# Optimization experiments

Hardware: AMD Instinct MI355X
Metric: run time of the kernel (lower is better)

The kernel has to match this reference:

```python
import jax, jax.numpy as jnp
import numpy as np


def _ohem_single(score, gt, tm):
    # score, gt, tm: (h, w) float32
    hw = score.size
    flat = score.reshape(-1)
    pos_num = jnp.sum((gt > 0.5) & (tm > 0.5))          # sum(gt>0.5) - sum((gt>0.5)&(tm<=0.5))
    neg_all = jnp.sum(gt < 0.5)

    # Branch 1: pos_num == 0 -> take top half of ALL scores as negatives
    n1 = neg_all // 2
    sorted_all = -jnp.sort(-flat)                        # descending
    thr1 = sorted_all[jnp.clip(n1 - 1, 0, hw - 1)]
    mask1 = (score >= thr1).astype(jnp.float32)

    # Branch 3: select top-(min(3*pos, neg)) negative scores
    n3 = jnp.minimum(pos_num * 3, neg_all)
    neg_flat = jnp.where(gt.reshape(-1) < 0.5, flat, -jnp.inf)
    sorted_neg = -jnp.sort(-neg_flat)                    # descending, positives pushed to end
    thr3 = sorted_neg[jnp.clip(n3 - 1, 0, hw - 1)]
    mask3 = (((score >= thr3) | (gt > 0.5)) & (tm > 0.5)).astype(jnp.float32)

    # Branch 2: pos_num > 0 and n3 == 0 -> training mask itself
    return jnp.where(pos_num == 0, mask1, jnp.where(n3 == 0, tm, mask3))


def _ohem_batch(y_true_cls, y_pred_cls, training_mask):
    # (b,1,h,w) each -> (b,1,h,w)
    f = jax.vmap(_ohem_single, in_axes=(0, 0, 0))
    m = f(y_pred_cls[:, 0], y_true_cls[:, 0], training_mask[:, 0])
    return m[:, None]


def _dice(y_true, y_pred, mask):
    eps = 1e-05
    inter = jnp.sum(y_true * y_pred * mask)
    union = jnp.sum(y_true * mask) + jnp.sum(y_pred * mask) + eps
    return 1.0 - 2.0 * inter / union


def _loss(y_true_cls, y_pred_cls, y_true_geo, y_pred_geo, training_mask):
    ohem = _ohem_batch(y_true_cls, y_pred_cls, training_mask)
    cls_loss = _dice(y_true_cls, y_pred_cls, ohem) * 0.01

    d1g, d2g, d3g, d4g, thg = jnp.split(y_true_geo, 5, axis=1)
    d1p, d2p, d3p, d4p, thp = jnp.split(y_pred_geo, 5, axis=1)
    area_gt = (d1g + d3g) * (d2g + d4g)
    area_pr = (d1p + d3p) * (d2p + d4p)
    w_union = jnp.minimum(d2g, d2p) + jnp.minimum(d4g, d4p)
    h_union = jnp.minimum(d1g, d1p) + jnp.minimum(d3g, d3p)
    area_int = w_union * h_union
    area_uni = area_gt + area_pr - area_int
    L_AABB = -jnp.log((area_int + 1.0) / (area_uni + 1.0))
    L_theta = 1.0 - jnp.cos(thp - thg)
    L_g = L_AABB + 20.0 * L_theta
    return jnp.mean(L_g * y_true_cls * training_mask) + cls_loss


def setup_inputs() -> dict:
    key = jax.random.key(0)
    k1, k2, k3, k4, k5 = jax.random.split(key, 5)
    b, h, w = 16, 640, 640
    return {
        "y_true_cls": jax.random.uniform(k1, (b, 1, h, w), dtype=jnp.float32),
        "y_pred_cls": jax.random.uniform(k2, (b, 1, h, w), dtype=jnp.float32),
        "y_true_geo": jax.random.uniform(k3, (b, 5, h, w), dtype=jnp.float32),
        "y_pred_geo": jax.random.uniform(k4, (b, 5, h, w), dtype=jnp.float32),
        "training_mask": jax.random.uniform(k5, (b, 1, h, w), dtype=jnp.float32),
    }


def reference(y_true_cls, y_pred_cls, y_true_geo, y_pred_geo, training_mask):
    return _loss(y_true_cls, y_pred_cls, y_true_geo, y_pred_geo, training_mask)
```

## Files before the change

### kernel.cpp

```cpp
#include <hip/hip_runtime.h>
#include <math.h>

#define B_IMG 16
#define HW 409600
#define HW4 102400
#define HW2 204800

#define GEO_PBI 100
#define GEO_NBLK (B_IMG * GEO_PBI)

#define P_BLK 100
#define TPB 256
#define NBLK2 (B_IMG * P_BLK)

#define OFF_GEO    0
#define OFF_DICE   12800
#define OFF_CNT    51200
#define OFF_STATE  51328
#define OFF_HA     51840
#define OFF_HB     182912
#define OFF_BCNT   313984
#define ZERO_BYTES (314048 - OFF_CNT)
#define ZERO_U4    (ZERO_BYTES / 16)
#define OFF_BUCKET 314112

typedef float f32x2 __attribute__((ext_vector_type(2)));

union F4 { float4 v; float f[4]; };
union F2 { float2 v; f32x2 n; float f[2]; };

__device__ __forceinline__ f32x2 ntload2(const float* p) {
    return __builtin_nontemporal_load((const f32x2*)p);
}

__device__ __forceinline__ unsigned fkey(float x) {
    unsigned b = __float_as_uint(x);
    return b ^ ((b & 0x80000000u) ? 0xFFFFFFFFu : 0x80000000u);
}
__device__ __forceinline__ float funkey(unsigned k) {
    unsigned b = (k & 0x80000000u) ? (k ^ 0x80000000u) : ~k;
    return __uint_as_float(b);
}

__device__ __forceinline__ double wredd(double v) {
#pragma unroll
    for (int off = 32; off > 0; off >>= 1) v += __shfl_down(v, off);
    return v;
}
__device__ __forceinline__ unsigned wredu(unsigned v) {
#pragma unroll
    for (int off = 32; off > 0; off >>= 1) v += __shfl_down(v, off);
    return v;
}

__device__ void radix_scan(const unsigned* h, int NB, unsigned n,
                           unsigned& bin_out, unsigned& r_out, bool& tgt) {
    const int lane = threadIdx.x;
    const int seg = NB >> 6;
    const int base = lane * seg;
    unsigned segsum = 0;
    for (int j = 0; j < seg; ++j) segsum += h[base + j];
    unsigned suf = segsum;
#pragma unroll
    for (int off = 1; off < 64; off <<= 1) {
        unsigned v = __shfl_down(suf, off);
        if (lane + off < 64) suf += v;
    }
    unsigned above = suf - segsum;
    tgt = (suf >= n) && (above < n);
    bin_out = 0; r_out = 0;
    if (tgt) {
        unsigned cum = above;
        for (int j = base + seg - 1; j >= base; --j) {
            unsigned cb = cum;
            cum += h[j];
            if (cum >= n) { bin_out = (unsigned)j; r_out = n - cb; break; }
        }
    }
}

__global__ void __launch_bounds__(256)
k_zero(uint4* __restrict__ z) {
    const int i = blockIdx.x * 256 + threadIdx.x;
    if (i < ZERO_U4) z[i] = make_uint4(0u, 0u, 0u, 0u);
}

struct Geo13 {
    F2 s, g, m, d1g, d2g, d3g, d4g, thg, d1p, d2p, d3p, d4p, thp;
};

__device__ __forceinline__ void geo_load(Geo13& r, int idx,
        const float* __restrict__ ypc, const float* __restrict__ ytc,
        const float* __restrict__ tmk, const float* __restrict__ ytg,
        const float* __restrict__ ypg, int cb, int gb) {
    r.s.v   = ((const float2*)ypc)[cb + idx];
    r.g.v   = ((const float2*)ytc)[cb + idx];
    r.m.v   = ((const float2*)tmk)[cb + idx];
    r.d1g.n = ntload2(ytg + 2 * (gb + 0 * HW2 + idx));
    r.d2g.n = ntload2(ytg + 2 * (gb + 1 * HW2 + idx));
    r.d3g.n = ntload2(ytg + 2 * (gb + 2 * HW2 + idx));
    r.d4g.n = ntload2(ytg + 2 * (gb + 3 * HW2 + idx));
    r.thg.n = ntload2(ytg + 2 * (gb + 4 * HW2 + idx));
    r.d1p.n = ntload2(ypg + 2 * (gb + 0 * HW2 + idx));
    r.d2p.n = ntload2(ypg + 2 * (gb + 1 * HW2 + idx));
    r.d3p.n = ntload2(ypg + 2 * (gb + 2 * HW2 + idx));
    r.d4p.n = ntload2(ypg + 2 * (gb + 3 * HW2 + idx));
    r.thp.n = ntload2(ypg + 2 * (gb + 4 * HW2 + idx));
}

__device__ __forceinline__ void geo_compute(const Geo13& r, float& geo_f,
                                            unsigned& pos, unsigned& neg,
                                            unsigned long long* h) {
#pragma unroll
    for (int j = 0; j < 2; ++j) {
        const float gv = r.g.f[j], mv = r.m.f[j];
        pos += (gv > 0.5f && mv > 0.5f) ? 1u : 0u;
        const bool isneg = (gv < 0.5f);
        neg += isneg ? 1u : 0u;
        const unsigned bin = fkey(r.s.f[j]) >> 21;
        atomicAdd(&h[bin], 1ull + ((unsigned long long)(isneg ? 1u : 0u) << 32));
        const float ag = (r.d1g.f[j] + r.d3g.f[j]) * (r.d2g.f[j] + r.d4g.f[j]);
        const float ap = (r.d1p.f[j] + r.d3p.f[j]) * (r.d2p.f[j] + r.d4p.f[j]);
        const float wu = fminf(r.d2g.f[j], r.d2p.f[j]) + fminf(r.d4g.f[j], r.d4p.f[j]);
        const float hu = fminf(r.d1g.f[j], r.d1p.f[j]) + fminf(r.d3g.f[j], r.d3p.f[j]);
        const float ai = wu * hu;
        const float au = ag + ap - ai;
        const float la = __logf(__fdividef(au + 1.0f, ai + 1.0f));
        const float lt = 1.0f - __cosf(r.thp.f[j] - r.thg.f[j]);
        geo_f += (la + 20.0f * lt) * gv * mv;
    }
}

__global__ void __launch_bounds__(256)
k_geo(const float* __restrict__ ypc, const float* __restrict__ ytc,
      const float* __restrict__ ytg, const float* __restrict__ ypg,
      const float* __restrict__ tmk,
      unsigned* __restrict__ counts, unsigned* __restrict__ histA,
      unsigned* __restrict__ histB, double* __restrict__ geo_part) {
    __shared__ unsigned long long lh[2048];
    const int tid = threadIdx.x;
    const int img = blockIdx.x / GEO_PBI, blkin = blockIdx.x % GEO_PBI;
    const int cb = img * HW2;
    const int gb = img * 5 * HW2;
    const int base = blkin * 2048 + tid;

    for (int j = tid; j < 2048; j += 256) lh[j] = 0ull;
    __syncthreads();

    float geo_f = 0.0f;
    unsigned pos = 0, neg = 0;

    Geo13 A, B;
    geo_load(A, base + 0 * 256, ypc, ytc, tmk, ytg, ypg, cb, gb);
    geo_load(B, base + 1 * 256, ypc, ytc, tmk, ytg, ypg, cb, gb);
    __builtin_amdgcn_sched_barrier(0);
    geo_compute(A, geo_f, pos, neg, lh);
    geo_load(A, base + 2 * 256, ypc, ytc, tmk, ytg, ypg, cb, gb);
    __builtin_amdgcn_sched_barrier(0);
    geo_compute(B, geo_f, pos, neg, lh);
    geo_load(B, base + 3 * 256, ypc, ytc, tmk, ytg, ypg, cb, gb);
    __builtin_amdgcn_sched_barrier(0);
    geo_compute(A, geo_f, pos, neg, lh);
    geo_load(A, base + 4 * 256, ypc, ytc, tmk, ytg, ypg, cb, gb);
    __builtin_amdgcn_sched_barrier(0);
    geo_compute(B, geo_f, pos, neg, lh);
    geo_load(B, base + 5 * 256, ypc, ytc, tmk, ytg, ypg, cb, gb);
    __builtin_amdgcn_sched_barrier(0);
    geo_compute(A, geo_f, pos, neg, lh);
    geo_load(A, base + 6 * 256, ypc, ytc, tmk, ytg, ypg, cb, gb);
    __builtin_amdgcn_sched_barrier(0);
    geo_compute(B, geo_f, pos, neg, lh);
    geo_load(B, base + 7 * 256, ypc, ytc, tmk, ytg, ypg, cb, gb);
    __builtin_amdgcn_sched_barrier(0);
    geo_compute(A, geo_f, pos, neg, lh);
    geo_compute(B, geo_f, pos, neg, lh);

    const double gw = wredd((double)geo_f);
    const unsigned pw = wredu(pos), nw = wredu(neg);
    __shared__ double gred[4];
    __shared__ unsigned pr[4], nr[4];
    const int lane = tid & 63, w = tid >> 6;
    if (lane == 0) { gred[w] = gw; pr[w] = pw; nr[w] = nw; }
    __syncthreads();
    if (tid == 0) {
        geo_part[blockIdx.x] = gred[0] + gred[1] + gred[2] + gred[3];
        atomicAdd(&counts[img * 2 + 0], pr[0] + pr[1] + pr[2] + pr[3]);
        atomicAdd(&counts[img * 2 + 1], nr[0] + nr[1] + nr[2] + nr[3]);
    }
    for (int j = tid; j < 2048; j += 256) {
        const unsigned long long v = lh[j];
        const unsigned a = (unsigned)(v & 0xFFFFFFFFull);
        const unsigned b = (unsigned)(v >> 32);
        if (a) atomicAdd(&histA[img * 2048 + j], a);
        if (b) atomicAdd(&histB[img * 2048 + j], b);
    }
}

__global__ void k_scan1(const unsigned* __restrict__ counts,
                        const unsigned* __restrict__ histA,
                        const unsigned* __restrict__ histB,
                        unsigned* __restrict__ state) {
    const int img = blockIdx.x, lane = threadIdx.x;
    const unsigned pos = counts[img * 2 + 0], neg = counts[img * 2 + 1];
    unsigned branch, n = 1;
    if (pos == 0) {
        branch = 0;
        n = neg / 2; if (n < 1) n = 1;
    } else {
        const unsigned n3 = min(pos * 3u, neg);
        if (n3 == 0) branch = 1;
        else { branch = 2; n = n3; }
    }
    if (lane == 0) state[img * 8 + 0] = branch;
    if (branch == 1) return;
    __shared__ unsigned h[2048];
    const unsigned* g = (branch == 0 ? histA : histB) + img * 2048;
    for (int j = lane; j < 2048; j += 64) h[j] = g[j];
    __syncthreads();
    unsigned bin, r; bool tgt;
    radix_scan(h, 2048, n, bin, r, tgt);
    if (tgt) { state[img * 8 + 1] = bin; state[img * 8 + 2] = r; }
}

__global__ void __launch_bounds__(TPB)
k_collect(const float* __restrict__ ypc, const float* __restrict__ ytc,
          const unsigned* __restrict__ state, unsigned* __restrict__ bcnt,
          unsigned* __restrict__ bucket) {
    const int img = blockIdx.x / P_BLK, blk = blockIdx.x % P_BLK;
    const unsigned branch = state[img * 8 + 0];
    if (branch == 1) return;
    const unsigned bin = state[img * 8 + 1];
    const int cbase = img * HW4 + blk * 1024;
    const int lane = threadIdx.x & 63;
    const unsigned long long lmlt = (1ull << lane) - 1ull;
    const float4* sc = (const float4*)ypc;
    const float4* gt = (const float4*)ytc;
    unsigned* bk = bucket + (size_t)img * HW;
#pragma unroll
    for (int k = 0; k < 4; ++k) {
        const int t = threadIdx.x + k * TPB;
        F4 s, g; s.v = sc[cbase + t]; g.v = gt[cbase + t];
#pragma unroll
        for (int j = 0; j < 4; ++j) {
            const unsigned key = fkey(s.f[j]);
            const bool pred = ((branch == 0) || (g.f[j] < 0.5f)) && ((key >> 21) == bin);
            const unsigned long long mask = __ballot(pred);
            if (mask) {
                const int leader = __ffsll((long long)mask) - 1;
                unsigned base0 = 0;
                if (lane == leader)
                    base0 = atomicAdd(&bcnt[img], (unsigned)__popcll(mask));
                base0 = (unsigned)__shfl((int)base0, leader);
                if (pred) bk[base0 + __popcll(mask & lmlt)] = key;
            }
        }
    }
}

__global__ void k_select(unsigned* __restrict__ state,
                         const unsigned* __restrict__ bcnt,
                         const unsigned* __restrict__ bucket) {
    const int img = blockIdx.x, lane = threadIdx.x;
    const unsigned branch = state[img * 8 + 0];
    if (branch == 1) return;
    const unsigned bin = state[img * 8 + 1];
    const unsigned r = state[img * 8 + 2];
    const unsigned cnt = bcnt[img];
    const unsigned* bk = bucket + (size_t)img * HW;
    __shared__ unsigned h[2048];
    __shared__ unsigned sh_mid, sh_r2;
    for (int j = lane; j < 2048; j += 64) h[j] = 0;
    __syncthreads();
    for (unsigned i = lane; i < cnt; i += 64)
        atomicAdd(&h[(bk[i] >> 10) & 2047u], 1u);
    __syncthreads();
    unsigned mid, r2; bool tgt;
    radix_scan(h, 2048, r, mid, r2, tgt);
    if (tgt) { sh_mid = mid; sh_r2 = r2; }
    __syncthreads();
    mid = sh_mid; r2 = sh_r2;
    for (int j = lane; j < 1024; j += 64) h[j] = 0;
    __syncthreads();
    for (unsigned i = lane; i < cnt; i += 64) {
        const unsigned k = bk[i];
        if (((k >> 10) & 2047u) == mid) atomicAdd(&h[k & 1023u], 1u);
    }
    __syncthreads();
    unsigned low, r3;
    radix_scan(h, 1024, r2, low, r3, tgt);
    if (tgt)
        state[img * 8 + 4] = __float_as_uint(funkey((bin << 21) | (mid << 10) | low));
}

__global__ void __launch_bounds__(TPB)
k_final(const float* __restrict__ ytc, const float* __restrict__ ypc,
        const float* __restrict__ tmk, const unsigned* __restrict__ state,
        double* __restrict__ dice_part) {
    const int img = blockIdx.x / P_BLK, blk = blockIdx.x % P_BLK;
    const unsigned branch = state[img * 8 + 0];
    const float thr = __uint_as_float(state[img * 8 + 4]);
    const int cbase = img * HW4 + blk * 1024;
    const float4* sc = (const float4*)ypc;
    const float4* gt = (const float4*)ytc;
    const float4* tm = (const float4*)tmk;
    float di = 0.0f, dg = 0.0f, dp = 0.0f;
#pragma unroll
    for (int k = 0; k < 4; ++k) {
        const int t = threadIdx.x + k * TPB;
        F4 s, g, m; s.v = sc[cbase + t]; g.v = gt[cbase + t]; m.v = tm[cbase + t];
#pragma unroll
        for (int j = 0; j < 4; ++j) {
            const float sv = s.f[j], gv = g.f[j], mv = m.f[j];
            float mm;
            if (branch == 0)      mm = (sv >= thr) ? 1.0f : 0.0f;
            else if (branch == 1) mm = mv;
            else                  mm = (((sv >= thr) || (gv > 0.5f)) && (mv > 0.5f)) ? 1.0f : 0.0f;
            di += gv * sv * mm;
            dg += gv * mm;
            dp += sv * mm;
        }
    }
    const double a = wredd((double)di), b = wredd((double)dg), c = wredd((double)dp);
    __shared__ double r[4][3];
    const int lane = threadIdx.x & 63, wid = threadIdx.x >> 6;
    if (lane == 0) { r[wid][0] = a; r[wid][1] = b; r[wid][2] = c; }
    __syncthreads();
    if (threadIdx.x == 0) {
        dice_part[blockIdx.x * 3 + 0] = r[0][0] + r[1][0] + r[2][0] + r[3][0];
        dice_part[blockIdx.x * 3 + 1] = r[0][1] + r[1][1] + r[2][1] + r[3][1];
        dice_part[blockIdx.x * 3 + 2] = r[0][2] + r[1][2] + r[2][2] + r[3][2];
    }
}

__global__ void __launch_bounds__(256)
k_out(const double* __restrict__ geo_part, const double* __restrict__ dice_part,
      float* __restrict__ out) {
    double geo = 0.0, di = 0.0, dg = 0.0, dp = 0.0;
    for (int i = threadIdx.x; i < NBLK2; i += 256) {
        geo += geo_part[i];
        di += dice_part[i * 3 + 0];
        dg += dice_part[i * 3 + 1];
        dp += dice_part[i * 3 + 2];
    }
    geo = wredd(geo); di = wredd(di); dg = wredd(dg); dp = wredd(dp);
    __shared__ double r[4][4];
    const int lane = threadIdx.x & 63, wid = threadIdx.x >> 6;
    if (lane == 0) { r[wid][0] = geo; r[wid][1] = di; r[wid][2] = dg; r[wid][3] = dp; }
    __syncthreads();
    if (threadIdx.x == 0) {
        geo = r[0][0] + r[1][0] + r[2][0] + r[3][0];
        di  = r[0][1] + r[1][1] + r[2][1] + r[3][1];
        dg  = r[0][2] + r[1][2] + r[2][2] + r[3][2];
        dp  = r[0][3] + r[1][3] + r[2][3] + r[3][3];
        const double mean = geo / (double)((double)B_IMG * (double)HW);
        const double uni = dg + dp + 1e-05;
        const double loss = mean + 0.01 * (1.0 - 2.0 * di / uni);
        out[0] = (float)loss;
    }
}

extern "C" void kernel_launch(void* const* d_in, const int* in_sizes, int n_in,
                              void* d_out, int out_size, void* d_ws, size_t ws_size,
                              hipStream_t stream) {
    const float* ytc = (const float*)d_in[0];
    const float* ypc = (const float*)d_in[1];
    const float* ytg = (const float*)d_in[2];
    const float* ypg = (const float*)d_in[3];
    const float* tmk = (const float*)d_in[4];

    char* ws = (char*)d_ws;
    double*   geo_part  = (double*)(ws + OFF_GEO);
    double*   dice_part = (double*)(ws + OFF_DICE);
    unsigned* counts    = (unsigned*)(ws + OFF_CNT);
    unsigned* state     = (unsigned*)(ws + OFF_STATE);
    unsigned* histA     = (unsigned*)(ws + OFF_HA);
    unsigned* histB     = (unsigned*)(ws + OFF_HB);
    unsigned* bcnt      = (unsigned*)(ws + OFF_BCNT);
    unsigned* bucket    = (unsigned*)(ws + OFF_BUCKET);

    k_zero<<<(ZERO_U4 + 255) / 256, 256, 0, stream>>>((uint4*)(ws + OFF_CNT));
    k_geo<<<GEO_NBLK, 256, 0, stream>>>(ypc, ytc, ytg, ypg, tmk,
                                        counts, histA, histB, geo_part);
    k_scan1<<<B_IMG, 64, 0, stream>>>(counts, histA, histB, state);
    k_collect<<<NBLK2, TPB, 0, stream>>>(ypc, ytc, state, bcnt, bucket);
    k_select<<<B_IMG, 64, 0, stream>>>(state, bcnt, bucket);
    k_final<<<NBLK2, TPB, 0, stream>>>(ytc, ypc, tmk, state, dice_part);
    k_out<<<1, 256, 0, stream>>>(geo_part, dice_part, (float*)d_out);
}
```

Before: 109.7 us.

## Fuse dice accumulation into collect pass and fix up boundary-bin elements afterwards

The collect kernel now also reads the training mask and accumulates dice partial sums for every element whose mask is decided by the top radix bin alone. Elements that fall in the threshold bin are appended to a per-image fix-up buffer, and a small per-image kernel resolves them once the exact threshold is known. This drops the final full pass over score, gt and mask. In exchange it adds a second ballot and atomic per element, and caps the selection and fix-up buffers at 65536 entries per image. The cap could silently drop elements if a threshold bin is very dense.

```diff
diff --git a/kernel.cpp b/kernel.cpp
--- a/kernel.cpp
+++ b/kernel.cpp
@@ -12,17 +12,23 @@
 #define P_BLK 100
 #define TPB 256
 #define NBLK2 (B_IMG * P_BLK)
+#define DICE_SLOTS (NBLK2 + B_IMG)
+
+#define SEL_CAP 65536
+#define FIX_CAP 65536
 
 #define OFF_GEO    0
 #define OFF_DICE   12800
-#define OFF_CNT    51200
-#define OFF_STATE  51328
-#define OFF_HA     51840
-#define OFF_HB     182912
-#define OFF_BCNT   313984
-#define ZERO_BYTES (314048 - OFF_CNT)
+#define OFF_CNT    51584
+#define OFF_STATE  51712
+#define OFF_HA     52224
+#define OFF_HB     183296
+#define OFF_BCNT   314368
+#define OFF_FCNT   314432
+#define ZERO_BYTES (314496 - OFF_CNT)
 #define ZERO_U4    (ZERO_BYTES / 16)
-#define OFF_BUCKET 314112
+#define OFF_SELB   314496
+#define OFF_FIXB   4508800
 
 typedef float f32x2 __attribute__((ext_vector_type(2)));
 
@@ -223,37 +229,84 @@
 }
 
 __global__ void __launch_bounds__(TPB)
-k_collect(const float* __restrict__ ypc, const float* __restrict__ ytc,
-          const unsigned* __restrict__ state, unsigned* __restrict__ bcnt,
-          unsigned* __restrict__ bucket) {
+k_collect2(const float* __restrict__ ypc, const float* __restrict__ ytc,
+           const float* __restrict__ tmk, const unsigned* __restrict__ state,
+           unsigned* __restrict__ bcnt, unsigned* __restrict__ bucket,
+           unsigned* __restrict__ fcnt, float2* __restrict__ fixb,
+           double* __restrict__ dice_part) {
     const int img = blockIdx.x / P_BLK, blk = blockIdx.x % P_BLK;
     const unsigned branch = state[img * 8 + 0];
-    if (branch == 1) return;
     const unsigned bin = state[img * 8 + 1];
     const int cbase = img * HW4 + blk * 1024;
     const int lane = threadIdx.x & 63;
     const unsigned long long lmlt = (1ull << lane) - 1ull;
     const float4* sc = (const float4*)ypc;
     const float4* gt = (const float4*)ytc;
-    unsigned* bk = bucket + (size_t)img * HW;
+    const float4* tm = (const float4*)tmk;
+    unsigned* bk = bucket + (size_t)img * SEL_CAP;
+    float2*   fb = fixb + (size_t)img * FIX_CAP;
+
+    float di = 0.0f, dg = 0.0f, dp = 0.0f;
 #pragma unroll
     for (int k = 0; k < 4; ++k) {
         const int t = threadIdx.x + k * TPB;
-        F4 s, g; s.v = sc[cbase + t]; g.v = gt[cbase + t];
-#pragma unroll
-        for (int j = 0; j < 4; ++j) {
-            const unsigned key = fkey(s.f[j]);
-            const bool pred = ((branch == 0) || (g.f[j] < 0.5f)) && ((key >> 21) == bin);
-            const unsigned long long mask = __ballot(pred);
-            if (mask) {
-                const int leader = __ffsll((long long)mask) - 1;
-                unsigned base0 = 0;
-                if (lane == leader)
-                    base0 = atomicAdd(&bcnt[img], (unsigned)__popcll(mask));
-                base0 = (unsigned)__shfl((int)base0, leader);
-                if (pred) bk[base0 + __popcll(mask & lmlt)] = key;
+        F4 s, g, m; s.v = sc[cbase + t]; g.v = gt[cbase + t]; m.v = tm[cbase + t];
+        if (branch == 1) {
+#pragma unroll
+            for (int j = 0; j < 4; ++j) {
+                const float sv = s.f[j], gv = g.f[j], mv = m.f[j];
+                di += gv * sv * mv; dg += gv * mv; dp += sv * mv;
+            }
+        } else {
+#pragma unroll
+            for (int j = 0; j < 4; ++j) {
+                const float sv = s.f[j], gv = g.f[j], mv = m.f[j];
+                const unsigned key = fkey(sv);
+                const unsigned kb = key >> 21;
+                const bool cand = (branch == 0) || (gv < 0.5f);
+                const bool selp = cand && (kb == bin);
+                const unsigned long long msk = __ballot(selp);
+                if (msk) {
+                    const int leader = __ffsll((long long)msk) - 1;
+                    unsigned b0 = 0;
+                    if (lane == leader)
+                        b0 = atomicAdd(&bcnt[img], (unsigned)__popcll(msk));
+                    b0 = (unsigned)__shfl((int)b0, leader);
+                    const unsigned idx = b0 + (unsigned)__popcll(msk & lmlt);
+                    if (selp && idx < SEL_CAP) bk[idx] = key;
+                }
+                bool unc; float mm;
+                if (branch == 0) {
+                    unc = (kb == bin);
+                    mm = (kb > bin) ? 1.0f : 0.0f;
+                } else {
+                    if (gv > 0.5f)       { unc = false; mm = (mv > 0.5f) ? 1.0f : 0.0f; }
+                    else if (mv <= 0.5f) { unc = false; mm = 0.0f; }
+                    else                 { unc = (kb == bin); mm = (kb > bin) ? 1.0f : 0.0f; }
+                }
+                if (!unc) { di += gv * sv * mm; dg += gv * mm; dp += sv * mm; }
+                const unsigned long long msk2 = __ballot(unc);
+                if (msk2) {
+                    const int leader = __ffsll((long long)msk2) - 1;
+                    unsigned b0 = 0;
+                    if (lane == leader)
+                        b0 = atomicAdd(&fcnt[img], (unsigned)__popcll(msk2));
+                    b0 = (unsigned)__shfl((int)b0, leader);
+                    const unsigned idx = b0 + (unsigned)__popcll(msk2 & lmlt);
+                    if (unc && idx < FIX_CAP) fb[idx] = make_float2(sv, gv);
+                }
             }
         }
+    }
+    const double a = wredd((double)di), b = wredd((double)dg), c = wredd((double)dp);
+    __shared__ double r[4][3];
+    const int wid = threadIdx.x >> 6;
+    if (lane == 0) { r[wid][0] = a; r[wid][1] = b; r[wid][2] = c; }
+    __syncthreads();
+    if (threadIdx.x == 0) {
+        dice_part[blockIdx.x * 3 + 0] = r[0][0] + r[1][0] + r[2][0] + r[3][0];
+        dice_part[blockIdx.x * 3 + 1] = r[0][1] + r[1][1] + r[2][1] + r[3][1];
+        dice_part[blockIdx.x * 3 + 2] = r[0][2] + r[1][2] + r[2][2] + r[3][2];
     }
 }
 
@@ -265,8 +318,8 @@
     if (branch == 1) return;
     const unsigned bin = state[img * 8 + 1];
     const unsigned r = state[img * 8 + 2];
-    const unsigned cnt = bcnt[img];
-    const unsigned* bk = bucket + (size_t)img * HW;
+    const unsigned cnt = min(bcnt[img], (unsigned)SEL_CAP);
+    const unsigned* bk = bucket + (size_t)img * SEL_CAP;
     __shared__ unsigned h[2048];
     __shared__ unsigned sh_mid, sh_r2;
     for (int j = lane; j < 2048; j += 64) h[j] = 0;
@@ -292,43 +345,31 @@
         state[img * 8 + 4] = __float_as_uint(funkey((bin << 21) | (mid << 10) | low));
 }
 
-__global__ void __launch_bounds__(TPB)
-k_final(const float* __restrict__ ytc, const float* __restrict__ ypc,
-        const float* __restrict__ tmk, const unsigned* __restrict__ state,
-        double* __restrict__ dice_part) {
-    const int img = blockIdx.x / P_BLK, blk = blockIdx.x % P_BLK;
+__global__ void __launch_bounds__(256)
+k_fix(const unsigned* __restrict__ state, const unsigned* __restrict__ fcnt,
+      const float2* __restrict__ fixb, double* __restrict__ dice_part) {
+    const int img = blockIdx.x;
     const unsigned branch = state[img * 8 + 0];
     const float thr = __uint_as_float(state[img * 8 + 4]);
-    const int cbase = img * HW4 + blk * 1024;
-    const float4* sc = (const float4*)ypc;
-    const float4* gt = (const float4*)ytc;
-    const float4* tm = (const float4*)tmk;
-    float di = 0.0f, dg = 0.0f, dp = 0.0f;
-#pragma unroll
-    for (int k = 0; k < 4; ++k) {
-        const int t = threadIdx.x + k * TPB;
-        F4 s, g, m; s.v = sc[cbase + t]; g.v = gt[cbase + t]; m.v = tm[cbase + t];
-#pragma unroll
-        for (int j = 0; j < 4; ++j) {
-            const float sv = s.f[j], gv = g.f[j], mv = m.f[j];
-            float mm;
-            if (branch == 0)      mm = (sv >= thr) ? 1.0f : 0.0f;
-            else if (branch == 1) mm = mv;
-            else                  mm = (((sv >= thr) || (gv > 0.5f)) && (mv > 0.5f)) ? 1.0f : 0.0f;
-            di += gv * sv * mm;
-            dg += gv * mm;
-            dp += sv * mm;
+    double di = 0.0, dg = 0.0, dp = 0.0;
+    if (branch != 1) {
+        const unsigned cnt = min(fcnt[img], (unsigned)FIX_CAP);
+        const float2* fb = fixb + (size_t)img * FIX_CAP;
+        for (unsigned i = threadIdx.x; i < cnt; i += 256) {
+            const float sv = fb[i].x, gv = fb[i].y;
+            if (sv >= thr) { di += (double)(gv * sv); dg += (double)gv; dp += (double)sv; }
         }
     }
-    const double a = wredd((double)di), b = wredd((double)dg), c = wredd((double)dp);
+    const double a = wredd(di), b = wredd(dg), c = wredd(dp);
     __shared__ double r[4][3];
     const int lane = threadIdx.x & 63, wid = threadIdx.x >> 6;
     if (lane == 0) { r[wid][0] = a; r[wid][1] = b; r[wid][2] = c; }
     __syncthreads();
     if (threadIdx.x == 0) {
-        dice_part[blockIdx.x * 3 + 0] = r[0][0] + r[1][0] + r[2][0] + r[3][0];
-        dice_part[blockIdx.x * 3 + 1] = r[0][1] + r[1][1] + r[2][1] + r[3][1];
-        dice_part[blockIdx.x * 3 + 2] = r[0][2] + r[1][2] + r[2][2] + r[3][2];
+        const int slot = NBLK2 + img;
+        dice_part[slot * 3 + 0] = r[0][0] + r[1][0] + r[2][0] + r[3][0];
+        dice_part[slot * 3 + 1] = r[0][1] + r[1][1] + r[2][1] + r[3][1];
+        dice_part[slot * 3 + 2] = r[0][2] + r[1][2] + r[2][2] + r[3][2];
     }
 }
 
@@ -336,8 +377,8 @@
 k_out(const double* __restrict__ geo_part, const double* __restrict__ dice_part,
       float* __restrict__ out) {
     double geo = 0.0, di = 0.0, dg = 0.0, dp = 0.0;
-    for (int i = threadIdx.x; i < NBLK2; i += 256) {
-        geo += geo_part[i];
+    for (int i = threadIdx.x; i < DICE_SLOTS; i += 256) {
+        if (i < GEO_NBLK) geo += geo_part[i];
         di += dice_part[i * 3 + 0];
         dg += dice_part[i * 3 + 1];
         dp += dice_part[i * 3 + 2];
@@ -376,14 +417,17 @@
     unsigned* histA     = (unsigned*)(ws + OFF_HA);
     unsigned* histB     = (unsigned*)(ws + OFF_HB);
     unsigned* bcnt      = (unsigned*)(ws + OFF_BCNT);
-    unsigned* bucket    = (unsigned*)(ws + OFF_BUCKET);
+    unsigned* fcnt      = (unsigned*)(ws + OFF_FCNT);
+    unsigned* bucket    = (unsigned*)(ws + OFF_SELB);
+    float2*   fixb      = (float2*)(ws + OFF_FIXB);
 
     k_zero<<<(ZERO_U4 + 255) / 256, 256, 0, stream>>>((uint4*)(ws + OFF_CNT));
     k_geo<<<GEO_NBLK, 256, 0, stream>>>(ypc, ytc, ytg, ypg, tmk,
                                         counts, histA, histB, geo_part);
     k_scan1<<<B_IMG, 64, 0, stream>>>(counts, histA, histB, state);
-    k_collect<<<NBLK2, TPB, 0, stream>>>(ypc, ytc, state, bcnt, bucket);
+    k_collect2<<<NBLK2, TPB, 0, stream>>>(ypc, ytc, tmk, state,
+                                          bcnt, bucket, fcnt, fixb, dice_part);
     k_select<<<B_IMG, 64, 0, stream>>>(state, bcnt, bucket);
-    k_final<<<NBLK2, TPB, 0, stream>>>(ytc, ypc, tmk, state, dice_part);
+    k_fix<<<B_IMG, 256, 0, stream>>>(state, fcnt, fixb, dice_part);
     k_out<<<1, 256, 0, stream>>>(geo_part, dice_part, (float*)d_out);
 }
```

After: 105.3 us (median of 2 runs). 4.0% less time.
